# Kernel optimization log

Measured on AMD Instinct MI355X. Metric: run time of the kernel, lower is better.

## Reference

```python
import jax, jax.numpy as jnp
import numpy as np

B, L, Q = 1024, 200, 1
DQ, DF = 512, 128
H, D1, D2 = 4, 128, 64


def setup_inputs() -> dict:
    key = jax.random.key(0)
    ks = jax.random.split(key, 20)
    inp = {
        "query": jax.random.normal(ks[0], (B, Q, DQ), jnp.float32),
        "fact": jax.random.normal(ks[1], (B, L, DF), jnp.float32),
        "mask": jax.random.randint(ks[2], (B, L), 0, 2, jnp.int32),
        "mm_cosine": jax.random.normal(ks[3], (2, B, L), jnp.float32),
    }
    # per-head FCRepeat weights, init per reset_parameters: randn/sqrt(fan_in), bias 0.1
    def w(k, fan_in, fan_out):
        return jax.random.normal(k, (H, fan_in, fan_out), jnp.float32) / np.sqrt(fan_in).astype(np.float32)
    inp["Wq1"] = w(ks[4], DQ, D1); inp["bq1"] = jnp.full((H, D1), 0.1, jnp.float32)
    inp["Wq2"] = w(ks[5], D1, D2); inp["bq2"] = jnp.full((H, D2), 0.1, jnp.float32)
    inp["Wf1"] = w(ks[6], DF, D1); inp["bf1"] = jnp.full((H, D1), 0.1, jnp.float32)
    inp["Wf2"] = w(ks[7], D1, D2); inp["bf2"] = jnp.full((H, D2), 0.1, jnp.float32)
    inp["Wv1"] = w(ks[8], DF, D1); inp["bv1"] = jnp.full((H, D1), 0.1, jnp.float32)
    inp["Wv2"] = w(ks[9], D1, D2); inp["bv2"] = jnp.full((H, D2), 0.1, jnp.float32)
    inp["tau1"] = jnp.full((2, H), 0.1, jnp.float32)   # cosine_tau1
    inp["tau2"] = jnp.full((3, H), 1.0, jnp.float32)   # cosine_tau2
    return inp


def _silu(x):
    return x * jax.nn.sigmoid(x)


def reference(query, fact, mask, mm_cosine,
              Wq1, bq1, Wq2, bq2, Wf1, bf1, Wf2, bf2, Wv1, bv1, Wv2, bv2,
              tau1, tau2):
    # per-head FC stacks (identity acts inside FCRepeat), then SiLU gating
    fq = jnp.einsum('bqi,hio->hbqo', query, Wq1) + bq1[:, None, None, :]
    fq = jnp.einsum('hbqi,hio->hbqo', fq, Wq2) + bq2[:, None, None, :]
    fq = _silu(fq)                                   # [H,B,1,D2]
    ff = jnp.einsum('bli,hio->hblo', fact, Wf1) + bf1[:, None, None, :]
    ff = jnp.einsum('hbli,hio->hblo', ff, Wf2) + bf2[:, None, None, :]
    ff = _silu(ff)                                   # [H,B,L,D2]
    fv = jnp.einsum('bli,hio->hblo', fact, Wv1) + bv1[:, None, None, :]
    fv = jnp.einsum('hbli,hio->hblo', fv, Wv2) + bv2[:, None, None, :]
    fv = _silu(fv)                                   # [H,B,L,D2]

    dot = jnp.einsum('hbld,hbqd->hblq', ff, fq)      # [H,B,L,1]
    dot = dot + (-1e9) * (1.0 - mask.astype(jnp.float32))[None, :, :, None]

    # cosine-bias cross terms
    bias = (mm_cosine[0][None] / tau1[0][:, None, None]
            + mm_cosine[1][None] / tau1[1][:, None, None])[..., None]  # [H,B,L,1]
    b1, b2, b3 = (tau2[i][:, None, None, None] for i in range(3))
    dot = b1 * dot + b2 * bias + b3 * dot * bias

    alphas = jax.nn.softmax(dot, axis=2) + 1e-7      # softmax over L
    out = jnp.einsum('hbld,hblq->hbdq', fv, alphas)[..., 0]  # [H,B,D2]
    return jnp.transpose(out, (1, 0, 2)).reshape(out.shape[1], -1)  # [B,H*D2]
```

## Files before the change

### kernel.cpp

```cpp
#include <hip/hip_runtime.h>
#include <hip/hip_bf16.h>

typedef __attribute__((ext_vector_type(8))) short short8;
typedef __attribute__((ext_vector_type(4))) float f32x4;

#define NH   4
#define NB   1024
#define NL   200
#define NDQ  512
#define NDF  128
#define ND1  128
#define ND2  64
#define KP   136
#define NW   13
#define NT   (NW*64)

#define OFF_WQC   0
#define OFF_BQC   (NH*NDQ*ND2*4)
#define OFF_FQ    (OFF_BQC + NH*ND2*4)
#define OFF_WIMG  (OFF_FQ + NH*NB*ND2*4)
#define OFF_BFC   (OFF_WIMG + NH*3*ND2*KP*2)
#define OFF_BVC   (OFF_BFC + NH*ND2*4)

__device__ inline short f2bf(float f) {
    union { float f; unsigned u; } v; v.f = f;
    unsigned r = (v.u + 0x7FFFu + ((v.u >> 16) & 1u)) >> 16;
    return (short)r;
}
__device__ inline float bf2f(short s) {
    union { unsigned u; float f; } v; v.u = ((unsigned)(unsigned short)s) << 16;
    return v.f;
}
__device__ inline float fsilu(float z) {
    return z * __fdividef(1.f, 1.f + __expf(-z));
}

__global__ __launch_bounds__(256) void k_combine(
    const float* __restrict__ Wq1, const float* __restrict__ bq1,
    const float* __restrict__ Wq2, const float* __restrict__ bq2,
    const float* __restrict__ Wf1, const float* __restrict__ bf1,
    const float* __restrict__ Wf2, const float* __restrict__ bf2,
    const float* __restrict__ Wv1, const float* __restrict__ bv1,
    const float* __restrict__ Wv2, const float* __restrict__ bv2,
    float* __restrict__ WQC, float* __restrict__ BQC,
    __hip_bfloat16* __restrict__ WIMG, float* __restrict__ BFC, float* __restrict__ BVC)
{
    int g = blockIdx.x * 256 + threadIdx.x;
    if (g < NH*NDQ*ND2) {
        int h = g >> 15, r = g & 32767, i = r >> 6, j = r & 63;
        const float* a  = Wq1 + (h*NDQ + i)*ND1;
        const float* bb = Wq2 + h*ND1*ND2 + j;
        float s = 0.f;
        for (int k = 0; k < ND1; ++k) s += a[k] * bb[k*ND2];
        WQC[(h*NDQ + i)*ND2 + j] = s;
        return;
    }
    g -= NH*NDQ*ND2;
    if (g < 2*NH*NDF*ND2) {
        int which = (g >= NH*NDF*ND2);
        int r0 = g & (NH*NDF*ND2 - 1);
        int h = r0 >> 13, r = r0 & 8191, i = r >> 6, j = r & 63;
        const float* W1 = (which ? Wv1 : Wf1) + (h*NDF + i)*ND1;
        const float* W2 = (which ? Wv2 : Wf2) + h*ND1*ND2 + j;
        float s = 0.f;
        for (int k = 0; k < ND1; ++k) s += W1[k] * W2[k*ND2];
        short hi = f2bf(s);
        short lo = f2bf(s - bf2f(hi));
        __hip_bfloat16* img = WIMG + (size_t)((h*3 + (which ? 2 : 0))*ND2 + j)*KP + i;
        ((short*)img)[0] = hi;
        if (!which) ((short*)img)[ND2*KP] = lo;
        return;
    }
    g -= 2*NH*NDF*ND2;
    if (g < NH*ND2) {
        int h = g >> 6, j = g & 63;
        float s = bq2[h*ND2 + j];
        for (int k = 0; k < ND1; ++k) s += bq1[h*ND1 + k] * Wq2[(h*ND1 + k)*ND2 + j];
        BQC[g] = s; return;
    }
    g -= NH*ND2;
    if (g < NH*ND2) {
        int h = g >> 6, j = g & 63;
        float s = bf2[h*ND2 + j];
        for (int k = 0; k < ND1; ++k) s += bf1[h*ND1 + k] * Wf2[(h*ND1 + k)*ND2 + j];
        BFC[g] = s; return;
    }
    g -= NH*ND2;
    if (g < NH*ND2) {
        int h = g >> 6, j = g & 63;
        float s = bv2[h*ND2 + j];
        for (int k = 0; k < ND1; ++k) s += bv1[h*ND1 + k] * Wv2[(h*ND1 + k)*ND2 + j];
        BVC[g] = s; return;
    }
}

__global__ __launch_bounds__(256) void k_fq(
    const float* __restrict__ query, const float* __restrict__ WQC,
    const float* __restrict__ BQC, float* __restrict__ FQ)
{
    __shared__ __align__(16) float qS[2*NDQ];
    const int t = threadIdx.x;
    const int b0 = blockIdx.x * 2;
    {
        const float4* src = (const float4*)(query + (size_t)b0 * NDQ);
        ((float4*)qS)[t] = src[t];
    }
    __syncthreads();
    const int h = t >> 6, d = t & 63;
    float s0, s1;
    s0 = s1 = BQC[h*ND2 + d];
    const float* wp = WQC + (size_t)h*NDQ*ND2 + d;
    #pragma unroll 16
    for (int i = 0; i < NDQ; ++i) {
        float wv = wp[i*ND2];
        s0 += qS[i]       * wv;
        s1 += qS[NDQ + i] * wv;
    }
    float* o = FQ + ((size_t)h*NB + b0)*ND2 + d;
    o[0]   = fsilu(s0);
    o[ND2] = fsilu(s1);
}

__global__ __launch_bounds__(NT) void k_main(
    const float* __restrict__ fact,
    const int* __restrict__ mask,
    const float* __restrict__ mmc,
    const float* __restrict__ tau1,
    const float* __restrict__ tau2,
    const float* __restrict__ FQ,
    const float* __restrict__ BFC,
    const float* __restrict__ BVC,
    const __hip_bfloat16* __restrict__ WIMG,
    float* __restrict__ out)
{
    __shared__ __align__(16) __hip_bfloat16 wS[3*ND2*KP];
    __shared__ __align__(16) float pS[NW][132];

    const int t    = threadIdx.x;
    const int b    = blockIdx.x;
    const int w    = t >> 6;
    const int lane = t & 63;
    const int a15  = lane & 15;
    const int quad = lane >> 4;
    const bool act = (w < NW);

    const int bL = b * NL;

    short8 afh[4], afl[4];
    const short8 zero8 = {0,0,0,0,0,0,0,0};
    {
        int row = w*16 + a15;
        for (int kk = 0; kk < 4; ++kk) {
            short8 vh = zero8, vl = zero8;
            if (act && row < NL) {
                const float* p = fact + ((size_t)(bL + row))*NDF + kk*32 + quad*8;
                float4 x0 = *(const float4*)p;
                float4 x1 = *(const float4*)(p + 4);
                float v[8] = {x0.x, x0.y, x0.z, x0.w, x1.x, x1.y, x1.z, x1.w};
                for (int j = 0; j < 8; ++j) {
                    short hs = f2bf(v[j]);
                    vh[j] = hs;
                    vl[j] = f2bf(v[j] - bf2f(hs));
                }
            }
            afh[kk] = vh;
            afl[kk] = vl;
        }
    }

    float mkv[4], c0v[4], c1v[4];
    {
        int rbase = w*16 + quad*4;
        for (int rg = 0; rg < 4; ++rg) {
            int r = rbase + rg;
            if (act && r < NL) {
                mkv[rg] = 1e9f * (1.0f - (float)mask[bL + r]);
                c0v[rg] = mmc[bL + r];
                c1v[rg] = mmc[NB*NL + bL + r];
            } else { mkv[rg] = 0.f; c0v[rg] = 0.f; c1v[rg] = 0.f; }
        }
    }

    const f32x4 zf = {0.f, 0.f, 0.f, 0.f};

    {
        const float4* src = (const float4*)(WIMG);
        float4* dst = (float4*)wS;
        for (int i = t; i < 3264; i += NT) dst[i] = src[i];
    }
    __syncthreads();

    for (int h = 0; h < NH; ++h) {
        const float rt1a = __fdividef(1.f, tau1[h]);
        const float rt1b = __fdividef(1.f, tau1[NH + h]);
        const float t20 = tau2[h];
        const float t21 = tau2[NH + h];
        const float t22 = tau2[2*NH + h];

        float fqv[4], bfcv[4];
        for (int nt = 0; nt < 4; ++nt) {
            int col = nt*16 + a15;
            fqv[nt]  = FQ[((size_t)h*NB + b)*ND2 + col];
            bfcv[nt] = BFC[h*ND2 + col];
        }

        f32x4 acc[4];
        for (int nt = 0; nt < 4; ++nt) acc[nt] = zf;
        if (act) {
            __builtin_amdgcn_s_setprio(1);
            for (int kk = 0; kk < 4; ++kk) {
                short8 bh[4], bl[4];
                for (int nt = 0; nt < 4; ++nt) {
                    const __hip_bfloat16* p = wS + (nt*16 + a15)*KP + kk*32 + quad*8;
                    bh[nt] = *(const short8*)p;
                    bl[nt] = *(const short8*)(p + ND2*KP);
                }
                for (int nt = 0; nt < 4; ++nt) {
                    acc[nt] = __builtin_amdgcn_mfma_f32_16x16x32_bf16(afh[kk], bh[nt], acc[nt], 0, 0, 0);
                    acc[nt] = __builtin_amdgcn_mfma_f32_16x16x32_bf16(afh[kk], bl[nt], acc[nt], 0, 0, 0);
                    acc[nt] = __builtin_amdgcn_mfma_f32_16x16x32_bf16(afl[kk], bh[nt], acc[nt], 0, 0, 0);
                }
            }
            __builtin_amdgcn_s_setprio(0);
        }

        float lg[4];
        for (int rg = 0; rg < 4; ++rg) {
            float l = -3.0e38f;
            if (act) {
                float s = 0.f;
                for (int nt = 0; nt < 4; ++nt)
                    s += fsilu(acc[nt][rg] + bfcv[nt]) * fqv[nt];
                s += __shfl_xor(s, 1);
                s += __shfl_xor(s, 2);
                s += __shfl_xor(s, 4);
                s += __shfl_xor(s, 8);
                int r = w*16 + quad*4 + rg;
                if (r < NL) {
                    float dv = s - mkv[rg];
                    float bias = c0v[rg]*rt1a + c1v[rg]*rt1b;
                    l = t20*dv + t21*bias + t22*dv*bias;
                }
            }
            lg[rg] = l;
        }

        float m = fmaxf(fmaxf(lg[0], lg[1]), fmaxf(lg[2], lg[3]));
        m = fmaxf(m, __shfl_xor(m, 16));
        m = fmaxf(m, __shfl_xor(m, 32));
        float sw = 0.f;
        for (int rg = 0; rg < 4; ++rg) {
            float p = __expf(lg[rg] - m);
            lg[rg] = p;
            sw += p;
        }
        sw += __shfl_xor(sw, 16);
        sw += __shfl_xor(sw, 32);

        for (int nt = 0; nt < 4; ++nt) acc[nt] = zf;
        if (act) {
            __builtin_amdgcn_s_setprio(1);
            for (int kk = 0; kk < 4; ++kk) {
                short8 bh[4];
                for (int nt = 0; nt < 4; ++nt)
                    bh[nt] = *(const short8*)(wS + (2*ND2 + nt*16 + a15)*KP + kk*32 + quad*8);
                for (int nt = 0; nt < 4; ++nt)
                    acc[nt] = __builtin_amdgcn_mfma_f32_16x16x32_bf16(afh[kk], bh[nt], acc[nt], 0, 0, 0);
            }
            __builtin_amdgcn_s_setprio(0);
        }

        float bvcv[4];
        for (int nt = 0; nt < 4; ++nt) bvcv[nt] = BVC[h*ND2 + nt*16 + a15];
        float oE[4] = {0.f,0.f,0.f,0.f}, oS[4] = {0.f,0.f,0.f,0.f};
        if (act)
            for (int rg = 0; rg < 4; ++rg) {
                float p = lg[rg];
                int r = w*16 + quad*4 + rg;
                float vm = (r < NL) ? 1.f : 0.f;
                for (int nt = 0; nt < 4; ++nt) {
                    float sv = fsilu(acc[nt][rg] + bvcv[nt]);
                    oE[nt] += p * sv;
                    oS[nt] += vm * sv;
                }
            }
        for (int nt = 0; nt < 4; ++nt) {
            oE[nt] += __shfl_xor(oE[nt], 16);
            oE[nt] += __shfl_xor(oE[nt], 32);
            oS[nt] += __shfl_xor(oS[nt], 16);
            oS[nt] += __shfl_xor(oS[nt], 32);
        }
        if (act) {
            if (lane == 0) { pS[w][0] = m; pS[w][1] = sw; }
            if (quad == 0)
                for (int nt = 0; nt < 4; ++nt) {
                    pS[w][2  + nt*16 + a15] = oE[nt];
                    pS[w][66 + nt*16 + a15] = oS[nt];
                }
        }
        __syncthreads();

        if (h + 1 < NH) {
            const float4* src = (const float4*)(WIMG + (size_t)((h+1)*3)*ND2*KP);
            float4* dst = (float4*)wS;
            for (int i = t; i < 3264; i += NT) dst[i] = src[i];
        }
        if (t < 64) {
            float M = pS[0][0];
            for (int ww = 1; ww < NW; ++ww) M = fmaxf(M, pS[ww][0]);
            float den = 0.f, num = 0.f, s1 = 0.f;
            for (int ww = 0; ww < NW; ++ww) {
                float e = __expf(pS[ww][0] - M);
                den += e * pS[ww][1];
                num += e * pS[ww][2 + t];
                s1  += pS[ww][66 + t];
            }
            out[(size_t)b*(NH*ND2) + h*ND2 + t] = num * __fdividef(1.f, den) + 1e-7f * s1;
        }
        __syncthreads();
    }
}

extern "C" void kernel_launch(void* const* d_in, const int* in_sizes, int n_in,
                              void* d_out, int out_size, void* d_ws, size_t ws_size,
                              hipStream_t stream) {
    const float* query = (const float*)d_in[0];
    const float* fact  = (const float*)d_in[1];
    const int*   maskp = (const int*)d_in[2];
    const float* mmc   = (const float*)d_in[3];
    const float* Wq1 = (const float*)d_in[4];
    const float* bq1 = (const float*)d_in[5];
    const float* Wq2 = (const float*)d_in[6];
    const float* bq2 = (const float*)d_in[7];
    const float* Wf1 = (const float*)d_in[8];
    const float* bf1 = (const float*)d_in[9];
    const float* Wf2 = (const float*)d_in[10];
    const float* bf2 = (const float*)d_in[11];
    const float* Wv1 = (const float*)d_in[12];
    const float* bv1 = (const float*)d_in[13];
    const float* Wv2 = (const float*)d_in[14];
    const float* bv2 = (const float*)d_in[15];
    const float* tau1 = (const float*)d_in[16];
    const float* tau2 = (const float*)d_in[17];

    char* ws = (char*)d_ws;
    float*          WQC  = (float*)(ws + OFF_WQC);
    float*          BQC  = (float*)(ws + OFF_BQC);
    float*          FQ   = (float*)(ws + OFF_FQ);
    __hip_bfloat16* WIMG = (__hip_bfloat16*)(ws + OFF_WIMG);
    float*          BFC  = (float*)(ws + OFF_BFC);
    float*          BVC  = (float*)(ws + OFF_BVC);

    k_combine<<<771, 256, 0, stream>>>(Wq1, bq1, Wq2, bq2, Wf1, bf1, Wf2, bf2,
                                       Wv1, bv1, Wv2, bv2, WQC, BQC, WIMG, BFC, BVC);
    k_fq<<<NB/2, 256, 0, stream>>>(query, WQC, BQC, FQ);
    k_main<<<NB, NT, 0, stream>>>(fact, maskp, mmc, tau1, tau2, FQ, BFC, BVC, WIMG,
                                  (float*)d_out);
}
```

Baseline: 349.3 us.

## Split main kernel into one block per batch-head with XCD-aware mapping

The main kernel now launches one block per (batch, head) pair instead of looping over all four heads inside each block. Block indices are swizzled so the four head-blocks for a given batch land on the same XCD, which should let the repeated reads of `fact` hit in L2. The weight image is no longer staged in LDS; MFMA B-operands are loaded straight from global memory, and the row padding (KP) drops from 136 to 128. This adds parallelism and removes the per-head LDS copy and barriers. In exchange, each head block reloads and re-splits the fact tile into bf16 hi/lo parts, and weight fetches depend on cache hits.

```diff
diff --git a/kernel.cpp b/kernel.cpp
--- a/kernel.cpp
+++ b/kernel.cpp
@@ -11,7 +11,7 @@
 #define NDF  128
 #define ND1  128
 #define ND2  64
-#define KP   136
+#define KP   128
 #define NW   13
 #define NT   (NW*64)
 
@@ -133,16 +133,18 @@
     const __hip_bfloat16* __restrict__ WIMG,
     float* __restrict__ out)
 {
-    __shared__ __align__(16) __hip_bfloat16 wS[3*ND2*KP];
     __shared__ __align__(16) float pS[NW][132];
 
     const int t    = threadIdx.x;
-    const int b    = blockIdx.x;
+    const int blk  = blockIdx.x;
+    const int x    = blk & 7;
+    const int i0   = blk >> 3;
+    const int b    = x * (NB/8) + (i0 >> 2);
+    const int h    = i0 & 3;
     const int w    = t >> 6;
     const int lane = t & 63;
     const int a15  = lane & 15;
     const int quad = lane >> 4;
-    const bool act = (w < NW);
 
     const int bL = b * NL;
 
@@ -152,7 +154,7 @@
         int row = w*16 + a15;
         for (int kk = 0; kk < 4; ++kk) {
             short8 vh = zero8, vl = zero8;
-            if (act && row < NL) {
+            if (row < NL) {
                 const float* p = fact + ((size_t)(bL + row))*NDF + kk*32 + quad*8;
                 float4 x0 = *(const float4*)p;
                 float4 x1 = *(const float4*)(p + 4);
@@ -173,7 +175,7 @@
         int rbase = w*16 + quad*4;
         for (int rg = 0; rg < 4; ++rg) {
             int r = rbase + rg;
-            if (act && r < NL) {
+            if (r < NL) {
                 mkv[rg] = 1e9f * (1.0f - (float)mask[bL + r]);
                 c0v[rg] = mmc[bL + r];
                 c1v[rg] = mmc[NB*NL + bL + r];
@@ -181,143 +183,120 @@
         }
     }
 
+    const float rt1a = __fdividef(1.f, tau1[h]);
+    const float rt1b = __fdividef(1.f, tau1[NH + h]);
+    const float t20 = tau2[h];
+    const float t21 = tau2[NH + h];
+    const float t22 = tau2[2*NH + h];
+
+    float fqv[4], bfcv[4];
+    for (int nt = 0; nt < 4; ++nt) {
+        int col = nt*16 + a15;
+        fqv[nt]  = FQ[((size_t)h*NB + b)*ND2 + col];
+        bfcv[nt] = BFC[h*ND2 + col];
+    }
+
     const f32x4 zf = {0.f, 0.f, 0.f, 0.f};
-
-    {
-        const float4* src = (const float4*)(WIMG);
-        float4* dst = (float4*)wS;
-        for (int i = t; i < 3264; i += NT) dst[i] = src[i];
-    }
+    const __hip_bfloat16* Wh = WIMG + (size_t)(h*3)*ND2*KP;
+
+    f32x4 acc[4];
+    for (int nt = 0; nt < 4; ++nt) acc[nt] = zf;
+    __builtin_amdgcn_s_setprio(1);
+    for (int kk = 0; kk < 4; ++kk) {
+        short8 bh[4], bl[4];
+        for (int nt = 0; nt < 4; ++nt) {
+            const __hip_bfloat16* p = Wh + (nt*16 + a15)*KP + kk*32 + quad*8;
+            bh[nt] = *(const short8*)p;
+            bl[nt] = *(const short8*)(p + ND2*KP);
+        }
+        for (int nt = 0; nt < 4; ++nt) {
+            acc[nt] = __builtin_amdgcn_mfma_f32_16x16x32_bf16(afh[kk], bh[nt], acc[nt], 0, 0, 0);
+            acc[nt] = __builtin_amdgcn_mfma_f32_16x16x32_bf16(afh[kk], bl[nt], acc[nt], 0, 0, 0);
+            acc[nt] = __builtin_amdgcn_mfma_f32_16x16x32_bf16(afl[kk], bh[nt], acc[nt], 0, 0, 0);
+        }
+    }
+    __builtin_amdgcn_s_setprio(0);
+
+    float lg[4];
+    for (int rg = 0; rg < 4; ++rg) {
+        float l = -3.0e38f;
+        float s = 0.f;
+        for (int nt = 0; nt < 4; ++nt)
+            s += fsilu(acc[nt][rg] + bfcv[nt]) * fqv[nt];
+        s += __shfl_xor(s, 1);
+        s += __shfl_xor(s, 2);
+        s += __shfl_xor(s, 4);
+        s += __shfl_xor(s, 8);
+        int r = w*16 + quad*4 + rg;
+        if (r < NL) {
+            float dv = s - mkv[rg];
+            float bias = c0v[rg]*rt1a + c1v[rg]*rt1b;
+            l = t20*dv + t21*bias + t22*dv*bias;
+        }
+        lg[rg] = l;
+    }
+
+    float m = fmaxf(fmaxf(lg[0], lg[1]), fmaxf(lg[2], lg[3]));
+    m = fmaxf(m, __shfl_xor(m, 16));
+    m = fmaxf(m, __shfl_xor(m, 32));
+    float sw = 0.f;
+    for (int rg = 0; rg < 4; ++rg) {
+        float p = __expf(lg[rg] - m);
+        lg[rg] = p;
+        sw += p;
+    }
+    sw += __shfl_xor(sw, 16);
+    sw += __shfl_xor(sw, 32);
+
+    for (int nt = 0; nt < 4; ++nt) acc[nt] = zf;
+    __builtin_amdgcn_s_setprio(1);
+    for (int kk = 0; kk < 4; ++kk) {
+        short8 bv[4];
+        for (int nt = 0; nt < 4; ++nt)
+            bv[nt] = *(const short8*)(Wh + (2*ND2 + nt*16 + a15)*KP + kk*32 + quad*8);
+        for (int nt = 0; nt < 4; ++nt)
+            acc[nt] = __builtin_amdgcn_mfma_f32_16x16x32_bf16(afh[kk], bv[nt], acc[nt], 0, 0, 0);
+    }
+    __builtin_amdgcn_s_setprio(0);
+
+    float bvcv[4];
+    for (int nt = 0; nt < 4; ++nt) bvcv[nt] = BVC[h*ND2 + nt*16 + a15];
+    float oE[4] = {0.f,0.f,0.f,0.f}, oS[4] = {0.f,0.f,0.f,0.f};
+    for (int rg = 0; rg < 4; ++rg) {
+        float p = lg[rg];
+        int r = w*16 + quad*4 + rg;
+        float vm = (r < NL) ? 1.f : 0.f;
+        for (int nt = 0; nt < 4; ++nt) {
+            float sv = fsilu(acc[nt][rg] + bvcv[nt]);
+            oE[nt] += p * sv;
+            oS[nt] += vm * sv;
+        }
+    }
+    for (int nt = 0; nt < 4; ++nt) {
+        oE[nt] += __shfl_xor(oE[nt], 16);
+        oE[nt] += __shfl_xor(oE[nt], 32);
+        oS[nt] += __shfl_xor(oS[nt], 16);
+        oS[nt] += __shfl_xor(oS[nt], 32);
+    }
+    if (lane == 0) { pS[w][0] = m; pS[w][1] = sw; }
+    if (quad == 0)
+        for (int nt = 0; nt < 4; ++nt) {
+            pS[w][2  + nt*16 + a15] = oE[nt];
+            pS[w][66 + nt*16 + a15] = oS[nt];
+        }
     __syncthreads();
 
-    for (int h = 0; h < NH; ++h) {
-        const float rt1a = __fdividef(1.f, tau1[h]);
-        const float rt1b = __fdividef(1.f, tau1[NH + h]);
-        const float t20 = tau2[h];
-        const float t21 = tau2[NH + h];
-        const float t22 = tau2[2*NH + h];
-
-        float fqv[4], bfcv[4];
-        for (int nt = 0; nt < 4; ++nt) {
-            int col = nt*16 + a15;
-            fqv[nt]  = FQ[((size_t)h*NB + b)*ND2 + col];
-            bfcv[nt] = BFC[h*ND2 + col];
-        }
-
-        f32x4 acc[4];
-        for (int nt = 0; nt < 4; ++nt) acc[nt] = zf;
-        if (act) {
-            __builtin_amdgcn_s_setprio(1);
-            for (int kk = 0; kk < 4; ++kk) {
-                short8 bh[4], bl[4];
-                for (int nt = 0; nt < 4; ++nt) {
-                    const __hip_bfloat16* p = wS + (nt*16 + a15)*KP + kk*32 + quad*8;
-                    bh[nt] = *(const short8*)p;
-                    bl[nt] = *(const short8*)(p + ND2*KP);
-                }
-                for (int nt = 0; nt < 4; ++nt) {
-                    acc[nt] = __builtin_amdgcn_mfma_f32_16x16x32_bf16(afh[kk], bh[nt], acc[nt], 0, 0, 0);
-                    acc[nt] = __builtin_amdgcn_mfma_f32_16x16x32_bf16(afh[kk], bl[nt], acc[nt], 0, 0, 0);
-                    acc[nt] = __builtin_amdgcn_mfma_f32_16x16x32_bf16(afl[kk], bh[nt], acc[nt], 0, 0, 0);
-                }
-            }
-            __builtin_amdgcn_s_setprio(0);
-        }
-
-        float lg[4];
-        for (int rg = 0; rg < 4; ++rg) {
-            float l = -3.0e38f;
-            if (act) {
-                float s = 0.f;
-                for (int nt = 0; nt < 4; ++nt)
-                    s += fsilu(acc[nt][rg] + bfcv[nt]) * fqv[nt];
-                s += __shfl_xor(s, 1);
-                s += __shfl_xor(s, 2);
-                s += __shfl_xor(s, 4);
-                s += __shfl_xor(s, 8);
-                int r = w*16 + quad*4 + rg;
-                if (r < NL) {
-                    float dv = s - mkv[rg];
-                    float bias = c0v[rg]*rt1a + c1v[rg]*rt1b;
-                    l = t20*dv + t21*bias + t22*dv*bias;
-                }
-            }
-            lg[rg] = l;
-        }
-
-        float m = fmaxf(fmaxf(lg[0], lg[1]), fmaxf(lg[2], lg[3]));
-        m = fmaxf(m, __shfl_xor(m, 16));
-        m = fmaxf(m, __shfl_xor(m, 32));
-        float sw = 0.f;
-        for (int rg = 0; rg < 4; ++rg) {
-            float p = __expf(lg[rg] - m);
-            lg[rg] = p;
-            sw += p;
-        }
-        sw += __shfl_xor(sw, 16);
-        sw += __shfl_xor(sw, 32);
-
-        for (int nt = 0; nt < 4; ++nt) acc[nt] = zf;
-        if (act) {
-            __builtin_amdgcn_s_setprio(1);
-            for (int kk = 0; kk < 4; ++kk) {
-                short8 bh[4];
-                for (int nt = 0; nt < 4; ++nt)
-                    bh[nt] = *(const short8*)(wS + (2*ND2 + nt*16 + a15)*KP + kk*32 + quad*8);
-                for (int nt = 0; nt < 4; ++nt)
-                    acc[nt] = __builtin_amdgcn_mfma_f32_16x16x32_bf16(afh[kk], bh[nt], acc[nt], 0, 0, 0);
-            }
-            __builtin_amdgcn_s_setprio(0);
-        }
-
-        float bvcv[4];
-        for (int nt = 0; nt < 4; ++nt) bvcv[nt] = BVC[h*ND2 + nt*16 + a15];
-        float oE[4] = {0.f,0.f,0.f,0.f}, oS[4] = {0.f,0.f,0.f,0.f};
-        if (act)
-            for (int rg = 0; rg < 4; ++rg) {
-                float p = lg[rg];
-                int r = w*16 + quad*4 + rg;
-                float vm = (r < NL) ? 1.f : 0.f;
-                for (int nt = 0; nt < 4; ++nt) {
-                    float sv = fsilu(acc[nt][rg] + bvcv[nt]);
-                    oE[nt] += p * sv;
-                    oS[nt] += vm * sv;
-                }
-            }
-        for (int nt = 0; nt < 4; ++nt) {
-            oE[nt] += __shfl_xor(oE[nt], 16);
-            oE[nt] += __shfl_xor(oE[nt], 32);
-            oS[nt] += __shfl_xor(oS[nt], 16);
-            oS[nt] += __shfl_xor(oS[nt], 32);
-        }
-        if (act) {
-            if (lane == 0) { pS[w][0] = m; pS[w][1] = sw; }
-            if (quad == 0)
-                for (int nt = 0; nt < 4; ++nt) {
-                    pS[w][2  + nt*16 + a15] = oE[nt];
-                    pS[w][66 + nt*16 + a15] = oS[nt];
-                }
-        }
-        __syncthreads();
-
-        if (h + 1 < NH) {
-            const float4* src = (const float4*)(WIMG + (size_t)((h+1)*3)*ND2*KP);
-            float4* dst = (float4*)wS;
-            for (int i = t; i < 3264; i += NT) dst[i] = src[i];
-        }
-        if (t < 64) {
-            float M = pS[0][0];
-            for (int ww = 1; ww < NW; ++ww) M = fmaxf(M, pS[ww][0]);
-            float den = 0.f, num = 0.f, s1 = 0.f;
-            for (int ww = 0; ww < NW; ++ww) {
-                float e = __expf(pS[ww][0] - M);
-                den += e * pS[ww][1];
-                num += e * pS[ww][2 + t];
-                s1  += pS[ww][66 + t];
-            }
-            out[(size_t)b*(NH*ND2) + h*ND2 + t] = num * __fdividef(1.f, den) + 1e-7f * s1;
-        }
-        __syncthreads();
+    if (t < 64) {
+        float M = pS[0][0];
+        for (int ww = 1; ww < NW; ++ww) M = fmaxf(M, pS[ww][0]);
+        float den = 0.f, num = 0.f, s1 = 0.f;
+        for (int ww = 0; ww < NW; ++ww) {
+            float e = __expf(pS[ww][0] - M);
+            den += e * pS[ww][1];
+            num += e * pS[ww][2 + t];
+            s1  += pS[ww][66 + t];
+        }
+        out[(size_t)b*(NH*ND2) + h*ND2 + t] = num * __fdividef(1.f, den) + 1e-7f * s1;
     }
 }
 
@@ -354,6 +333,6 @@
     k_combine<<<771, 256, 0, stream>>>(Wq1, bq1, Wq2, bq2, Wf1, bf1, Wf2, bf2,
                                        Wv1, bv1, Wv2, bv2, WQC, BQC, WIMG, BFC, BVC);
     k_fq<<<NB/2, 256, 0, stream>>>(query, WQC, BQC, FQ);
-    k_main<<<NB, NT, 0, stream>>>(fact, maskp, mmc, tau1, tau2, FQ, BFC, BVC, WIMG,
-                                  (float*)d_out);
-}
+    k_main<<<NB*NH, NT, 0, stream>>>(fact, maskp, mmc, tau1, tau2, FQ, BFC, BVC, WIMG,
+                                     (float*)d_out);
+}
```

Result: slower. 572.2 us (+63.8%).
